# Performance work log

Hardware: AMD Instinct MI355X
Metric: run time of the kernel (lower is better)

Reference implementation:

```python
import jax, jax.numpy as jnp
import numpy as np


def setup_inputs() -> dict:
    key = jax.random.key(0)
    k1, k2, k3, k4 = jax.random.split(key, 4)
    bs, num_feat, num_points = 1, 256, 8192
    return {
        "emb1": jax.random.normal(k1, (bs, num_feat, num_points), dtype=jnp.float32),
        "emb2": jax.random.normal(k2, (bs, num_feat, num_points), dtype=jnp.float32),
        "t1": jax.random.normal(k3, (bs, 3, num_points), dtype=jnp.float32),
        "t2": jax.random.normal(k4, (bs, 3, num_points), dtype=jnp.float32),
    }


def reference(emb1, emb2, t1, t2):
    bs, num_feat, num_points = emb1.shape
    t1 = t1.reshape(bs, 3, -1)  # [bs, 3, N1] reference points
    t2 = t2.reshape(bs, 3, -1)  # [bs, 3, N2] query points
    # Brute-force 1-NN: squared Euclidean distance [bs, N1, N2]
    d2 = (
        jnp.sum(t1 * t1, axis=1)[:, :, None]
        + jnp.sum(t2 * t2, axis=1)[:, None, :]
        - 2.0 * jnp.einsum("bdn,bdm->bnm", t1, t2)
    )
    inds = jnp.argmin(d2, axis=1)  # [bs, N2] index into reference points (0-based)
    # Gather nearest-neighbor embeddings from emb1 (indices are constants / detached)
    inds_b = jax.lax.stop_gradient(inds)[:, None, :]  # [bs, 1, N2]
    emb1_nn = jnp.take_along_axis(emb1, jnp.broadcast_to(inds_b, emb1.shape), axis=2)
    # stack([emb1, emb2], dim=1).view(bs, 2*num_feat, num_points) == concat on feat axis
    emb = jnp.concatenate([emb1_nn, emb2], axis=1)  # [bs, 2*num_feat, N2]
    return emb
```

## Files before the change

kernel.cpp:

```cpp
#include <hip/hip_runtime.h>
#include <hip/hip_bf16.h>

#define NPTS  8192
#define NFEAT 256
#define CHUNK 256
#define NCHUNK (NPTS / CHUNK)

#define WS_KEYS_OFF 0
#define WS_REF_OFF  65536

__global__ __launch_bounds__(256) void prep_kernel(const float* __restrict__ t1f,
                                                   float4* __restrict__ ref,
                                                   unsigned long long* __restrict__ keys) {
    int i = blockIdx.x * 256 + threadIdx.x;
    float x = t1f[i], y = t1f[NPTS + i], z = t1f[2 * NPTS + i];
    float n1 = __fadd_rn(__fadd_rn(__fmul_rn(x, x), __fmul_rn(y, y)), __fmul_rn(z, z));
    ref[i]  = make_float4(x, y, z, n1);
    keys[i] = ~0ULL;
}

__global__ __launch_bounds__(256) void argmin_kernel(const float* __restrict__ t2f,
                                                     const float4* __restrict__ ref,
                                                     unsigned long long* __restrict__ keys) {
    int j    = blockIdx.x * 256 + threadIdx.x;
    int base = blockIdx.y * CHUNK;

    float qx = t2f[j], qy = t2f[NPTS + j], qz = t2f[2 * NPTS + j];
    float n2 = __fadd_rn(__fadd_rn(__fmul_rn(qx, qx), __fmul_rn(qy, qy)), __fmul_rn(qz, qz));

    float inf = __int_as_float(0x7f800000);
    float b0 = inf, b1 = inf;
    int   i0 = base, i1 = base + 1;

    #pragma unroll 4
    for (int k = 0; k < CHUNK; k += 2) {
        float4 p = ref[base + k];
        float4 q = ref[base + k + 1];
        float dot0 = __fadd_rn(__fadd_rn(__fmul_rn(p.x, qx), __fmul_rn(p.y, qy)), __fmul_rn(p.z, qz));
        float d20  = __fsub_rn(__fadd_rn(p.w, n2), __fmul_rn(2.0f, dot0));
        float dot1 = __fadd_rn(__fadd_rn(__fmul_rn(q.x, qx), __fmul_rn(q.y, qy)), __fmul_rn(q.z, qz));
        float d21  = __fsub_rn(__fadd_rn(q.w, n2), __fmul_rn(2.0f, dot1));
        if (d20 < b0) { b0 = d20; i0 = base + k; }
        if (d21 < b1) { b1 = d21; i1 = base + k + 1; }
    }

    float best = b0; int idx = i0;
    if (b1 < b0 || (b1 == b0 && i1 < i0)) { best = b1; idx = i1; }

    unsigned ub = __float_as_uint(best);
    ub ^= ((unsigned)((int)ub >> 31)) | 0x80000000u;
    unsigned long long key = ((unsigned long long)ub << 13) | (unsigned)idx;
    atomicMin(keys + j, key);
}

__global__ __launch_bounds__(256) void gather_kernel(const float* __restrict__ emb1,
                                                     const float* __restrict__ emb2,
                                                     const unsigned long long* __restrict__ keys,
                                                     float* __restrict__ out) {
    int j0 = (blockIdx.x * 256 + threadIdx.x) * 4;
    int f  = blockIdx.y;
    float4 v;
    if (f < NFEAT) {
        const float* row = emb1 + (size_t)f * NPTS;
        v.x = row[(int)(keys[j0 + 0] & 8191ULL)];
        v.y = row[(int)(keys[j0 + 1] & 8191ULL)];
        v.z = row[(int)(keys[j0 + 2] & 8191ULL)];
        v.w = row[(int)(keys[j0 + 3] & 8191ULL)];
    } else {
        v = *(const float4*)(emb2 + (size_t)(f - NFEAT) * NPTS + j0);
    }
    *(float4*)(out + (size_t)f * NPTS + j0) = v;
}

extern "C" void kernel_launch(void* const* d_in, const int* in_sizes, int n_in,
                              void* d_out, int out_size, void* d_ws, size_t ws_size,
                              hipStream_t stream) {
    const float* emb1 = (const float*)d_in[0];
    const float* emb2 = (const float*)d_in[1];
    const float* t1   = (const float*)d_in[2];
    const float* t2   = (const float*)d_in[3];
    float* out = (float*)d_out;

    unsigned long long* keys = (unsigned long long*)((char*)d_ws + WS_KEYS_OFF);
    float4*             ref  = (float4*)((char*)d_ws + WS_REF_OFF);

    prep_kernel<<<dim3(NPTS / 256), 256, 0, stream>>>(t1, ref, keys);
    argmin_kernel<<<dim3(NPTS / 256, NCHUNK), 256, 0, stream>>>(t2, ref, keys);
    gather_kernel<<<dim3(NPTS / 1024, 2 * NFEAT), 256, 0, stream>>>(emb1, emb2, keys, out);
}
```

Measured before the change: 106.6 us.

## Stage reference chunk in LDS, two queries per thread, replace atomics with reduction

The argmin kernel now loads each 256-point reference chunk into shared memory, computing norms inline, so the separate prep kernel is gone. Each thread evaluates two queries per reference point, halving reference reads. Per-chunk results go to a partials buffer that a new reduce kernel min-reduces into 32-bit indices, replacing global 64-bit atomicMin. The gather then reads packed uint4 indices. In exchange it writes and rereads a 2 MB partials buffer and still needs three launches.

Result: no change. 106.5 us (-0.0%).

```diff
diff --git a/kernel.cpp b/kernel.cpp
--- a/kernel.cpp
+++ b/kernel.cpp
@@ -1,71 +1,90 @@
 #include <hip/hip_runtime.h>
-#include <hip/hip_bf16.h>
 
-#define NPTS  8192
-#define NFEAT 256
-#define CHUNK 256
-#define NCHUNK (NPTS / CHUNK)
+#define NPTS   8192
+#define NFEAT  256
+#define RCHUNK 256
+#define NCHUNK (NPTS / RCHUNK)
+#define QG     512
+#define NQG    (NPTS / QG)
 
-#define WS_KEYS_OFF 0
-#define WS_REF_OFF  65536
+#define WS_PART_OFF 0
+#define WS_IDX_OFF  (NCHUNK * NPTS * 8)
 
-__global__ __launch_bounds__(256) void prep_kernel(const float* __restrict__ t1f,
-                                                   float4* __restrict__ ref,
-                                                   unsigned long long* __restrict__ keys) {
-    int i = blockIdx.x * 256 + threadIdx.x;
-    float x = t1f[i], y = t1f[NPTS + i], z = t1f[2 * NPTS + i];
-    float n1 = __fadd_rn(__fadd_rn(__fmul_rn(x, x), __fmul_rn(y, y)), __fmul_rn(z, z));
-    ref[i]  = make_float4(x, y, z, n1);
-    keys[i] = ~0ULL;
+__device__ __forceinline__ unsigned long long pack_key(float d2, int idx) {
+    unsigned ub = __float_as_uint(d2);
+    ub ^= ((unsigned)((int)ub >> 31)) | 0x80000000u;
+    return ((unsigned long long)ub << 13) | (unsigned)idx;
 }
 
-__global__ __launch_bounds__(256) void argmin_kernel(const float* __restrict__ t2f,
-                                                     const float4* __restrict__ ref,
-                                                     unsigned long long* __restrict__ keys) {
-    int j    = blockIdx.x * 256 + threadIdx.x;
-    int base = blockIdx.y * CHUNK;
+__global__ __launch_bounds__(256) void argmin_kernel(const float* __restrict__ t1,
+                                                     const float* __restrict__ t2,
+                                                     unsigned long long* __restrict__ part) {
+#pragma clang fp contract(off)
+    __shared__ float4 sref[RCHUNK];
+    const int tid = threadIdx.x;
+    const int qg  = blockIdx.x;
+    const int rc  = blockIdx.y;
 
-    float qx = t2f[j], qy = t2f[NPTS + j], qz = t2f[2 * NPTS + j];
-    float n2 = __fadd_rn(__fadd_rn(__fmul_rn(qx, qx), __fmul_rn(qy, qy)), __fmul_rn(qz, qz));
+    {
+        int r = rc * RCHUNK + tid;
+        float x = t1[r], y = t1[NPTS + r], z = t1[2 * NPTS + r];
+        float n1 = (x * x + y * y) + z * z;
+        sref[tid] = make_float4(x, y, z, n1);
+    }
+    __syncthreads();
 
-    float inf = __int_as_float(0x7f800000);
+    const int j0 = qg * QG + tid;
+    const int j1 = j0 + 256;
+    float qx0 = t2[j0], qy0 = t2[NPTS + j0], qz0 = t2[2 * NPTS + j0];
+    float qx1 = t2[j1], qy1 = t2[NPTS + j1], qz1 = t2[2 * NPTS + j1];
+    float n20 = (qx0 * qx0 + qy0 * qy0) + qz0 * qz0;
+    float n21 = (qx1 * qx1 + qy1 * qy1) + qz1 * qz1;
+
+    const float inf = __int_as_float(0x7f800000);
     float b0 = inf, b1 = inf;
-    int   i0 = base, i1 = base + 1;
+    int   i0 = 0,   i1 = 0;
 
     #pragma unroll 4
-    for (int k = 0; k < CHUNK; k += 2) {
-        float4 p = ref[base + k];
-        float4 q = ref[base + k + 1];
-        float dot0 = __fadd_rn(__fadd_rn(__fmul_rn(p.x, qx), __fmul_rn(p.y, qy)), __fmul_rn(p.z, qz));
-        float d20  = __fsub_rn(__fadd_rn(p.w, n2), __fmul_rn(2.0f, dot0));
-        float dot1 = __fadd_rn(__fadd_rn(__fmul_rn(q.x, qx), __fmul_rn(q.y, qy)), __fmul_rn(q.z, qz));
-        float d21  = __fsub_rn(__fadd_rn(q.w, n2), __fmul_rn(2.0f, dot1));
-        if (d20 < b0) { b0 = d20; i0 = base + k; }
-        if (d21 < b1) { b1 = d21; i1 = base + k + 1; }
+    for (int k = 0; k < RCHUNK; ++k) {
+        float4 p = sref[k];
+        float dot0 = (p.x * qx0 + p.y * qy0) + p.z * qz0;
+        float d20  = (p.w + n20) - 2.0f * dot0;
+        float dot1 = (p.x * qx1 + p.y * qy1) + p.z * qz1;
+        float d21  = (p.w + n21) - 2.0f * dot1;
+        if (d20 < b0) { b0 = d20; i0 = k; }
+        if (d21 < b1) { b1 = d21; i1 = k; }
     }
 
-    float best = b0; int idx = i0;
-    if (b1 < b0 || (b1 == b0 && i1 < i0)) { best = b1; idx = i1; }
+    part[rc * NPTS + j0] = pack_key(b0, rc * RCHUNK + i0);
+    part[rc * NPTS + j1] = pack_key(b1, rc * RCHUNK + i1);
+}
 
-    unsigned ub = __float_as_uint(best);
-    ub ^= ((unsigned)((int)ub >> 31)) | 0x80000000u;
-    unsigned long long key = ((unsigned long long)ub << 13) | (unsigned)idx;
-    atomicMin(keys + j, key);
+__global__ __launch_bounds__(256) void reduce_kernel(const unsigned long long* __restrict__ part,
+                                                     unsigned* __restrict__ idx_out) {
+    int j = blockIdx.x * 256 + threadIdx.x;
+    unsigned long long m = part[j];
+    #pragma unroll
+    for (int s = 1; s < NCHUNK; ++s) {
+        unsigned long long k = part[s * NPTS + j];
+        m = k < m ? k : m;
+    }
+    idx_out[j] = (unsigned)(m & 8191ULL);
 }
 
 __global__ __launch_bounds__(256) void gather_kernel(const float* __restrict__ emb1,
                                                      const float* __restrict__ emb2,
-                                                     const unsigned long long* __restrict__ keys,
+                                                     const unsigned* __restrict__ idx,
                                                      float* __restrict__ out) {
     int j0 = (blockIdx.x * 256 + threadIdx.x) * 4;
     int f  = blockIdx.y;
     float4 v;
     if (f < NFEAT) {
         const float* row = emb1 + (size_t)f * NPTS;
-        v.x = row[(int)(keys[j0 + 0] & 8191ULL)];
-        v.y = row[(int)(keys[j0 + 1] & 8191ULL)];
-        v.z = row[(int)(keys[j0 + 2] & 8191ULL)];
-        v.w = row[(int)(keys[j0 + 3] & 8191ULL)];
+        uint4 id = *(const uint4*)(idx + j0);
+        v.x = row[id.x];
+        v.y = row[id.y];
+        v.z = row[id.z];
+        v.w = row[id.w];
     } else {
         v = *(const float4*)(emb2 + (size_t)(f - NFEAT) * NPTS + j0);
     }
@@ -81,10 +100,10 @@
     const float* t2   = (const float*)d_in[3];
     float* out = (float*)d_out;
 
-    unsigned long long* keys = (unsigned long long*)((char*)d_ws + WS_KEYS_OFF);
-    float4*             ref  = (float4*)((char*)d_ws + WS_REF_OFF);
+    unsigned long long* part = (unsigned long long*)((char*)d_ws + WS_PART_OFF);
+    unsigned*           idx  = (unsigned*)((char*)d_ws + WS_IDX_OFF);
 
-    prep_kernel<<<dim3(NPTS / 256), 256, 0, stream>>>(t1, ref, keys);
-    argmin_kernel<<<dim3(NPTS / 256, NCHUNK), 256, 0, stream>>>(t2, ref, keys);
-    gather_kernel<<<dim3(NPTS / 1024, 2 * NFEAT), 256, 0, stream>>>(emb1, emb2, keys, out);
+    argmin_kernel<<<dim3(NQG, NCHUNK), 256, 0, stream>>>(t1, t2, part);
+    reduce_kernel<<<dim3(NPTS / 256), 256, 0, stream>>>(part, idx);
+    gather_kernel<<<dim3(NPTS / 1024, 2 * NFEAT), 256, 0, stream>>>(emb1, emb2, idx, out);
 }
```
